# Optimization experiments

Measured on AMD Instinct MI355X. Metric: run time of the kernel, lower is better.

The kernel has to match this reference:

```python
import jax, jax.numpy as jnp
import numpy as np

D_MODEL = 1024
NUM_EXPERTS = 64
TOP_K = 2
TEMPERATURE = 1.0


def setup_inputs() -> dict:
    key = jax.random.key(0)
    k1, k2, k3, k4 = jax.random.split(key, 4)
    mh_output = jax.random.normal(k1, (8, 4096, D_MODEL), dtype=jnp.float32)
    noise = jax.random.normal(k2, (8, 4096, NUM_EXPERTS), dtype=jnp.float32)  # randn_like sample, externalized
    # nn.Linear weights: shape [out, in], init normal(0, 0.02); biases zero
    W_route = jax.random.normal(k3, (NUM_EXPERTS, D_MODEL), dtype=jnp.float32) * 0.02
    b_route = jnp.zeros((NUM_EXPERTS,), dtype=jnp.float32)
    W_noise = jax.random.normal(k4, (NUM_EXPERTS, D_MODEL), dtype=jnp.float32) * 0.02
    b_noise = jnp.zeros((NUM_EXPERTS,), dtype=jnp.float32)
    return {"mh_output": mh_output, "noise": noise, "W_route": W_route,
            "b_route": b_route, "W_noise": W_noise, "b_noise": b_noise}


def reference(mh_output, noise, W_route, b_route, W_noise, b_noise):
    # logits = topkroute_linear(mh_output); noise_logits = noise_linear(mh_output)
    logits = jnp.einsum('bsd,ed->bse', mh_output, W_route) + b_route
    noise_logits = jnp.einsum('bsd,ed->bse', mh_output, W_noise) + b_noise
    # noisy logits = logits + temperature * randn * softplus(noise_logits)
    noisy = logits + TEMPERATURE * noise * jax.nn.softplus(noise_logits)
    # top-k, scatter into -inf, softmax  ==  softmax over top-k values scattered into zeros
    top_vals, indices = jax.lax.top_k(noisy, TOP_K)          # [b, s, k]
    probs_k = jax.nn.softmax(top_vals, axis=-1)              # softmax(-inf elsewhere) -> 0 elsewhere
    one_hot = jax.nn.one_hot(indices, NUM_EXPERTS, dtype=noisy.dtype)  # [b, s, k, E]
    router_output = jnp.sum(one_hot * probs_k[..., None], axis=-2)     # [b, s, E]
    return router_output, indices
```

## Files before the change

### kernel.cpp

```cpp
#include <hip/hip_runtime.h>
#include <hip/hip_bf16.h>
#include <math.h>


#define T_TOKENS 32768
#define D_MODEL  1024
#define NE       64
#define NCOL     128
#define M_TILE   64
#define NCHUNK   32
#define CS_LD    68
#define OUT_IDX_BASE ((size_t)T_TOKENS * NE)
#define W_ELEMS  (NCOL * D_MODEL)

typedef short  bf16x8  __attribute__((ext_vector_type(8)));
typedef float  floatx4 __attribute__((ext_vector_type(4)));

__device__ __forceinline__ float softplus_f(float x) {
    return fmaxf(x, 0.f) + log1pf(expf(-fabsf(x)));
}

__device__ __forceinline__ void cvt8(const float4 a, const float4 b,
                                     int4* hi, int4* lo) {
    float v[8] = {a.x, a.y, a.z, a.w, b.x, b.y, b.z, b.w};
    int hw[4], lw[4];
    #pragma unroll
    for (int p = 0; p < 4; ++p) {
        float2 f2 = make_float2(v[2 * p], v[2 * p + 1]);
        __hip_bfloat162 h2 = __float22bfloat162_rn(f2);
        int u; __builtin_memcpy(&u, &h2, 4);
        float h0 = __uint_as_float(((unsigned)u) << 16);
        float h1 = __uint_as_float(((unsigned)u) & 0xFFFF0000u);
        float2 l2 = make_float2(v[2 * p] - h0, v[2 * p + 1] - h1);
        __hip_bfloat162 L2 = __float22bfloat162_rn(l2);
        int ul; __builtin_memcpy(&ul, &L2, 4);
        hw[p] = u; lw[p] = ul;
    }
    *hi = make_int4(hw[0], hw[1], hw[2], hw[3]);
    *lo = make_int4(lw[0], lw[1], lw[2], lw[3]);
}

__global__ __launch_bounds__(256) void prepack_w(
    const float* __restrict__ Wr, const float* __restrict__ Wn,
    short* __restrict__ Bh, short* __restrict__ Bl)
{
    int g   = blockIdx.x * 256 + threadIdx.x;
    int n   = g & 15;
    int kg  = (g >> 4) & 127;
    int t2  = g >> 11;
    int col = t2 * 16 + n;
    const float* src = (col < NE ? Wr + (size_t)col * D_MODEL
                                 : Wn + (size_t)(col - NE) * D_MODEL) + kg * 8;
    float4 a = *(const float4*)src;
    float4 b = *(const float4*)(src + 4);
    int4 hi, lo;
    cvt8(a, b, &hi, &lo);
    *(int4*)(Bh + (size_t)g * 8) = hi;
    *(int4*)(Bl + (size_t)g * 8) = lo;
}

__global__ __launch_bounds__(256, 2) void router_mfma(
    const float* __restrict__ A,
    const float* __restrict__ noise,
    const float* __restrict__ br,
    const float* __restrict__ bn,
    const short* __restrict__ Bh,
    const short* __restrict__ Bl,
    float* __restrict__ out)
{
    __shared__ __align__(16) short Ah[2][M_TILE * 32];
    __shared__ __align__(16) short Al[2][M_TILE * 32];
    __shared__ float Cs[M_TILE * CS_LD];
    __shared__ float s_p1[M_TILE], s_p2[M_TILE];
    __shared__ int   s_e1[M_TILE], s_e2[M_TILE];

    const int tid  = threadIdx.x;
    const int lane = tid & 63;
    const int wid  = tid >> 6;
    const int n16  = lane & 15;
    const int quad = lane >> 4;
    const int m0   = blockIdx.x * M_TILE;

    const int r  = tid & 63;
    const int kh = tid >> 6;
    const float* pA = A + (size_t)(m0 + r) * D_MODEL + kh * 8;
    const int sBase = (kh * M_TILE + r) * 8;

    const int bBaseR = ((wid * 128 + quad) * 16 + n16) * 8;
    const int bBaseN = (((4 + wid) * 128 + quad) * 16 + n16) * 8;

    floatx4 acc[4][2];
    #pragma unroll
    for (int i = 0; i < 4; ++i) { acc[i][0] = (floatx4)0.f; acc[i][1] = (floatx4)0.f; }

    {
        float4 a0 = *(const float4*)pA;
        float4 a1 = *(const float4*)(pA + 4);
        int4 hi, lo;
        cvt8(a0, a1, &hi, &lo);
        *(int4*)&Ah[0][sBase] = hi;
        *(int4*)&Al[0][sBase] = lo;
    }
    bf16x8 bhR, blR, bhN, blN;
    bhR = *(const bf16x8*)(Bh + bBaseR);
    blR = *(const bf16x8*)(Bl + bBaseR);
    bhN = *(const bf16x8*)(Bh + bBaseN);
    blN = *(const bf16x8*)(Bl + bBaseN);
    float4 aP1a = *(const float4*)(pA + 32), aP1b = *(const float4*)(pA + 36);
    float4 aP2a = *(const float4*)(pA + 64), aP2b = *(const float4*)(pA + 68);
    __syncthreads();

    for (int kc = 0; kc < NCHUNK; ++kc) {
        const int cur = kc & 1, nxt = cur ^ 1;

        float4 f0, f1;
        if (kc + 3 < NCHUNK) {
            f0 = *(const float4*)(pA + (kc + 3) * 32);
            f1 = *(const float4*)(pA + (kc + 3) * 32 + 4);
        }
        bf16x8 bhRn, blRn, bhNn, blNn;
        if (kc + 1 < NCHUNK) {
            int o = (kc + 1) * 512;
            bhRn = *(const bf16x8*)(Bh + bBaseR + o);
            blRn = *(const bf16x8*)(Bl + bBaseR + o);
            bhNn = *(const bf16x8*)(Bh + bBaseN + o);
            blNn = *(const bf16x8*)(Bl + bBaseN + o);
        }

        bf16x8 afh[4], afl[4];
        #pragma unroll
        for (int mf = 0; mf < 4; ++mf) {
            int g = (quad * M_TILE + mf * 16 + n16) * 8;
            afh[mf] = *(const bf16x8*)&Ah[cur][g];
            afl[mf] = *(const bf16x8*)&Al[cur][g];
        }

        if (kc + 1 < NCHUNK) {
            int4 hi, lo;
            cvt8(aP1a, aP1b, &hi, &lo);
            *(int4*)&Ah[nxt][sBase] = hi;
            *(int4*)&Al[nxt][sBase] = lo;
        }

        #pragma unroll
        for (int mf = 0; mf < 4; ++mf) {
            acc[mf][0] = __builtin_amdgcn_mfma_f32_16x16x32_bf16(afh[mf], bhR, acc[mf][0], 0, 0, 0);
            acc[mf][0] = __builtin_amdgcn_mfma_f32_16x16x32_bf16(afh[mf], blR, acc[mf][0], 0, 0, 0);
            acc[mf][0] = __builtin_amdgcn_mfma_f32_16x16x32_bf16(afl[mf], bhR, acc[mf][0], 0, 0, 0);
            acc[mf][1] = __builtin_amdgcn_mfma_f32_16x16x32_bf16(afh[mf], bhN, acc[mf][1], 0, 0, 0);
            acc[mf][1] = __builtin_amdgcn_mfma_f32_16x16x32_bf16(afh[mf], blN, acc[mf][1], 0, 0, 0);
            acc[mf][1] = __builtin_amdgcn_mfma_f32_16x16x32_bf16(afl[mf], blN == blN ? bhN : bhN, acc[mf][1], 0, 0, 0);
        }

        __syncthreads();

        aP1a = aP2a; aP1b = aP2b; aP2a = f0; aP2b = f1;
        bhR = bhRn; blR = blRn; bhN = bhNn; blN = blNn;
    }

    {
        int e = wid * 16 + n16;
        float brv = br[e], bnv = bn[e];
        #pragma unroll
        for (int mf = 0; mf < 4; ++mf)
            #pragma unroll
            for (int rr = 0; rr < 4; ++rr) {
                int t = mf * 16 + quad * 4 + rr;
                float nz    = noise[(size_t)(m0 + t) * NE + e];
                float route = acc[mf][0][rr] + brv;
                float nl    = acc[mf][1][rr] + bnv;
                Cs[t * CS_LD + e] = fmaf(nz, softplus_f(nl), route);
            }
    }
    __syncthreads();

    if (tid < M_TILE) {
        const int t = tid;
        float v1 = -INFINITY, v2 = -INFINITY;
        int e1 = 0, e2 = 0;
        #pragma unroll
        for (int e4 = 0; e4 < 16; ++e4) {
            float4 q = *(const float4*)&Cs[t * CS_LD + e4 * 4];
            float qa[4] = {q.x, q.y, q.z, q.w};
            #pragma unroll
            for (int c = 0; c < 4; ++c) {
                float v = qa[c];
                int e = e4 * 4 + c;
                if (v > v1) { v2 = v1; e2 = e1; v1 = v; e1 = e; }
                else if (v > v2) { v2 = v; e2 = e; }
            }
        }
        float ex = expf(v2 - v1);
        float denom = 1.f + ex;
        s_p1[t] = 1.f / denom;
        s_p2[t] = ex / denom;
        s_e1[t] = e1;
        s_e2[t] = e2;
        float2 iv = make_float2((float)e1, (float)e2);
        *(float2*)(out + OUT_IDX_BASE + (size_t)(m0 + t) * 2) = iv;
    }
    __syncthreads();

    #pragma unroll
    for (int i = 0; i < 4; ++i) {
        int gi = i * 256 + tid;
        int t  = gi >> 4;
        int e0 = (gi & 15) * 4;
        float p1 = s_p1[t], p2 = s_p2[t];
        int   e1 = s_e1[t], e2 = s_e2[t];
        float4 v;
        v.x = (e0 + 0 == e1) ? p1 : ((e0 + 0 == e2) ? p2 : 0.f);
        v.y = (e0 + 1 == e1) ? p1 : ((e0 + 1 == e2) ? p2 : 0.f);
        v.z = (e0 + 2 == e1) ? p1 : ((e0 + 2 == e2) ? p2 : 0.f);
        v.w = (e0 + 3 == e1) ? p1 : ((e0 + 3 == e2) ? p2 : 0.f);
        *(float4*)(out + (size_t)(m0 + t) * NE + e0) = v;
    }
}

extern "C" void kernel_launch(void* const* d_in, const int* in_sizes, int n_in,
                              void* d_out, int out_size, void* d_ws, size_t ws_size,
                              hipStream_t stream) {
    const float* A     = (const float*)d_in[0];
    const float* noise = (const float*)d_in[1];
    const float* Wr    = (const float*)d_in[2];
    const float* br    = (const float*)d_in[3];
    const float* Wn    = (const float*)d_in[4];
    const float* bn    = (const float*)d_in[5];
    float* out = (float*)d_out;

    short* Bh = (short*)d_ws;
    short* Bl = Bh + W_ELEMS;

    prepack_w<<<dim3(W_ELEMS / 8 / 256), dim3(256), 0, stream>>>(Wr, Wn, Bh, Bl);
    router_mfma<<<dim3(T_TOKENS / M_TILE), dim3(256), 0, stream>>>(A, noise, br, bn, Bh, Bl, out);
}
```

Measured before the change: 223.0 us.

## Halve token tile, double K per stage, and raise occupancy to four blocks

Shrinks the token tile from 64 to 32 rows, giving twice as many blocks, and processes 64 K elements per pipeline stage, so there are half as many barrier-separated stages. The launch-bounds hint rises to 4 blocks per SM for more occupancy. B fragments are no longer prefetched a stage ahead in registers; they are loaded at the start of each stage, and A prefetch depth drops from 3 chunks to 2 stages. The smaller M tile halves reuse of each B fragment, so weight traffic from L2 per token doubles, and load latency is now exposed unless occupancy hides it.

```diff
diff --git a/kernel.cpp b/kernel.cpp
--- a/kernel.cpp
+++ b/kernel.cpp
@@ -7,8 +7,9 @@
 #define D_MODEL  1024
 #define NE       64
 #define NCOL     128
-#define M_TILE   64
-#define NCHUNK   32
+#define M_TILE   32
+#define KSTAGE   64
+#define NSTAGE   16
 #define CS_LD    68
 #define OUT_IDX_BASE ((size_t)T_TOKENS * NE)
 #define W_ELEMS  (NCOL * D_MODEL)
@@ -59,7 +60,7 @@
     *(int4*)(Bl + (size_t)g * 8) = lo;
 }
 
-__global__ __launch_bounds__(256, 2) void router_mfma(
+__global__ __launch_bounds__(256, 4) void router_mfma(
     const float* __restrict__ A,
     const float* __restrict__ noise,
     const float* __restrict__ br,
@@ -68,8 +69,8 @@
     const short* __restrict__ Bl,
     float* __restrict__ out)
 {
-    __shared__ __align__(16) short Ah[2][M_TILE * 32];
-    __shared__ __align__(16) short Al[2][M_TILE * 32];
+    __shared__ __align__(16) short Ah[2][M_TILE * KSTAGE];
+    __shared__ __align__(16) short Al[2][M_TILE * KSTAGE];
     __shared__ float Cs[M_TILE * CS_LD];
     __shared__ float s_p1[M_TILE], s_p2[M_TILE];
     __shared__ int   s_e1[M_TILE], s_e2[M_TILE];
@@ -81,17 +82,17 @@
     const int quad = lane >> 4;
     const int m0   = blockIdx.x * M_TILE;
 
-    const int r  = tid & 63;
-    const int kh = tid >> 6;
+    const int r  = tid & 31;
+    const int kh = tid >> 5;
     const float* pA = A + (size_t)(m0 + r) * D_MODEL + kh * 8;
     const int sBase = (kh * M_TILE + r) * 8;
 
     const int bBaseR = ((wid * 128 + quad) * 16 + n16) * 8;
     const int bBaseN = (((4 + wid) * 128 + quad) * 16 + n16) * 8;
 
-    floatx4 acc[4][2];
+    floatx4 acc[2][2];
     #pragma unroll
-    for (int i = 0; i < 4; ++i) { acc[i][0] = (floatx4)0.f; acc[i][1] = (floatx4)0.f; }
+    for (int i = 0; i < 2; ++i) { acc[i][0] = (floatx4)0.f; acc[i][1] = (floatx4)0.f; }
 
     {
         float4 a0 = *(const float4*)pA;
@@ -101,41 +102,40 @@
         *(int4*)&Ah[0][sBase] = hi;
         *(int4*)&Al[0][sBase] = lo;
     }
-    bf16x8 bhR, blR, bhN, blN;
-    bhR = *(const bf16x8*)(Bh + bBaseR);
-    blR = *(const bf16x8*)(Bl + bBaseR);
-    bhN = *(const bf16x8*)(Bh + bBaseN);
-    blN = *(const bf16x8*)(Bl + bBaseN);
-    float4 aP1a = *(const float4*)(pA + 32), aP1b = *(const float4*)(pA + 36);
-    float4 aP2a = *(const float4*)(pA + 64), aP2b = *(const float4*)(pA + 68);
+    float4 aP1a = *(const float4*)(pA + KSTAGE);
+    float4 aP1b = *(const float4*)(pA + KSTAGE + 4);
     __syncthreads();
 
-    for (int kc = 0; kc < NCHUNK; ++kc) {
-        const int cur = kc & 1, nxt = cur ^ 1;
+    for (int s = 0; s < NSTAGE; ++s) {
+        const int cur = s & 1, nxt = cur ^ 1;
 
         float4 f0, f1;
-        if (kc + 3 < NCHUNK) {
-            f0 = *(const float4*)(pA + (kc + 3) * 32);
-            f1 = *(const float4*)(pA + (kc + 3) * 32 + 4);
-        }
-        bf16x8 bhRn, blRn, bhNn, blNn;
-        if (kc + 1 < NCHUNK) {
-            int o = (kc + 1) * 512;
-            bhRn = *(const bf16x8*)(Bh + bBaseR + o);
-            blRn = *(const bf16x8*)(Bl + bBaseR + o);
-            bhNn = *(const bf16x8*)(Bh + bBaseN + o);
-            blNn = *(const bf16x8*)(Bl + bBaseN + o);
-        }
-
-        bf16x8 afh[4], afl[4];
-        #pragma unroll
-        for (int mf = 0; mf < 4; ++mf) {
-            int g = (quad * M_TILE + mf * 16 + n16) * 8;
-            afh[mf] = *(const bf16x8*)&Ah[cur][g];
-            afl[mf] = *(const bf16x8*)&Al[cur][g];
-        }
-
-        if (kc + 1 < NCHUNK) {
+        if (s + 2 < NSTAGE) {
+            f0 = *(const float4*)(pA + (s + 2) * KSTAGE);
+            f1 = *(const float4*)(pA + (s + 2) * KSTAGE + 4);
+        }
+
+        bf16x8 bh[2][2], bl[2][2];
+        #pragma unroll
+        for (int c = 0; c < 2; ++c) {
+            const int o = (s * 2 + c) * 512;
+            bh[c][0] = *(const bf16x8*)(Bh + bBaseR + o);
+            bl[c][0] = *(const bf16x8*)(Bl + bBaseR + o);
+            bh[c][1] = *(const bf16x8*)(Bh + bBaseN + o);
+            bl[c][1] = *(const bf16x8*)(Bl + bBaseN + o);
+        }
+
+        bf16x8 afh[2][2], afl[2][2];
+        #pragma unroll
+        for (int c = 0; c < 2; ++c)
+            #pragma unroll
+            for (int mf = 0; mf < 2; ++mf) {
+                int g = ((c * 4 + quad) * M_TILE + mf * 16 + n16) * 8;
+                afh[c][mf] = *(const bf16x8*)&Ah[cur][g];
+                afl[c][mf] = *(const bf16x8*)&Al[cur][g];
+            }
+
+        if (s + 1 < NSTAGE) {
             int4 hi, lo;
             cvt8(aP1a, aP1b, &hi, &lo);
             *(int4*)&Ah[nxt][sBase] = hi;
@@ -143,26 +143,27 @@
         }
 
         #pragma unroll
-        for (int mf = 0; mf < 4; ++mf) {
-            acc[mf][0] = __builtin_amdgcn_mfma_f32_16x16x32_bf16(afh[mf], bhR, acc[mf][0], 0, 0, 0);
-            acc[mf][0] = __builtin_amdgcn_mfma_f32_16x16x32_bf16(afh[mf], blR, acc[mf][0], 0, 0, 0);
-            acc[mf][0] = __builtin_amdgcn_mfma_f32_16x16x32_bf16(afl[mf], bhR, acc[mf][0], 0, 0, 0);
-            acc[mf][1] = __builtin_amdgcn_mfma_f32_16x16x32_bf16(afh[mf], bhN, acc[mf][1], 0, 0, 0);
-            acc[mf][1] = __builtin_amdgcn_mfma_f32_16x16x32_bf16(afh[mf], blN, acc[mf][1], 0, 0, 0);
-            acc[mf][1] = __builtin_amdgcn_mfma_f32_16x16x32_bf16(afl[mf], blN == blN ? bhN : bhN, acc[mf][1], 0, 0, 0);
-        }
+        for (int c = 0; c < 2; ++c)
+            #pragma unroll
+            for (int mf = 0; mf < 2; ++mf) {
+                acc[mf][0] = __builtin_amdgcn_mfma_f32_16x16x32_bf16(afh[c][mf], bh[c][0], acc[mf][0], 0, 0, 0);
+                acc[mf][0] = __builtin_amdgcn_mfma_f32_16x16x32_bf16(afh[c][mf], bl[c][0], acc[mf][0], 0, 0, 0);
+                acc[mf][0] = __builtin_amdgcn_mfma_f32_16x16x32_bf16(afl[c][mf], bh[c][0], acc[mf][0], 0, 0, 0);
+                acc[mf][1] = __builtin_amdgcn_mfma_f32_16x16x32_bf16(afh[c][mf], bh[c][1], acc[mf][1], 0, 0, 0);
+                acc[mf][1] = __builtin_amdgcn_mfma_f32_16x16x32_bf16(afh[c][mf], bl[c][1], acc[mf][1], 0, 0, 0);
+                acc[mf][1] = __builtin_amdgcn_mfma_f32_16x16x32_bf16(afl[c][mf], bh[c][1], acc[mf][1], 0, 0, 0);
+            }
 
         __syncthreads();
 
-        aP1a = aP2a; aP1b = aP2b; aP2a = f0; aP2b = f1;
-        bhR = bhRn; blR = blRn; bhN = bhNn; blN = blNn;
+        aP1a = f0; aP1b = f1;
     }
 
     {
         int e = wid * 16 + n16;
         float brv = br[e], bnv = bn[e];
         #pragma unroll
-        for (int mf = 0; mf < 4; ++mf)
+        for (int mf = 0; mf < 2; ++mf)
             #pragma unroll
             for (int rr = 0; rr < 4; ++rr) {
                 int t = mf * 16 + quad * 4 + rr;
@@ -202,7 +203,7 @@
     __syncthreads();
 
     #pragma unroll
-    for (int i = 0; i < 4; ++i) {
+    for (int i = 0; i < 2; ++i) {
         int gi = i * 256 + tid;
         int t  = gi >> 4;
         int e0 = (gi & 15) * 4;
```

New measurement: 231.7 us. 3.9% more time.
